# Kernel optimization log

Measured on AMD Instinct MI355X. Metric: run time of the kernel, lower is better.

Reference implementation:

```python
import jax, jax.numpy as jnp
import numpy as np

B, O, M, H, E = 32, 64, 128, 4, 64  # batch, num_obj, memory_len, heads, embed


def setup_inputs() -> dict:
    key = jax.random.key(0)
    ks = jax.random.split(key, 10)
    s = 1.0 / np.sqrt(E)
    return {
        "query": jax.random.normal(ks[0], (B, O, E), jnp.float32),
        "context": jax.random.normal(ks[1], (B, M, E), jnp.float32),
        "memory": jax.random.normal(ks[2], (B, M, E), jnp.float32),
        "W_ch": jax.random.normal(ks[3], (E, H * E), jnp.float32) * s,
        "b_ch": jax.random.normal(ks[4], (H * E,), jnp.float32) * s,
        "w_logit": jax.random.normal(ks[5], (E,), jnp.float32) * s,
        "b_logit": jax.random.normal(ks[6], (1,), jnp.float32) * s,
        "W_rh": jax.random.normal(ks[7], (H * E, E), jnp.float32) * (1.0 / np.sqrt(H * E)),
        "b_rh": jax.random.normal(ks[8], (E,), jnp.float32) * (1.0 / np.sqrt(H * E)),
        "temp": jnp.float32(1.0),
    }


def reference(query, context, memory, W_ch, b_ch, w_logit, b_logit, W_rh, b_rh, temp):
    # create heads: [B,O,E] -> [B,O,H,E]
    q = (query @ W_ch + b_ch).reshape(B, O, H, E)
    # broadcast add query heads and context over memory axis: [B,O,M,H,E]
    qc = jnp.tanh(context[:, None, :, None, :] + q[:, :, None, :, :])
    # logit projection -> [B,O,M,H]
    logits = jnp.einsum("bomhe,e->bomh", qc, w_logit) + b_logit[0]
    # softmax over memory axis (dim=2)
    probs = jax.nn.softmax(logits / temp, axis=2)
    # weighted sum of memory over M: [B,O,H,E]
    heads = jnp.einsum("bomh,bme->bohe", probs, memory)
    heads = jax.nn.leaky_relu(heads, negative_slope=0.01)
    out = heads.reshape(B, O, H * E) @ W_rh + b_rh
    return out
```

## Files before the change

kernel.cpp:

```cpp
#include <hip/hip_runtime.h>
#include <hip/hip_fp16.h>

#define B 32
#define O 64
#define M 128
#define H 4
#define E 64
#define SC 2.88539008177792681f
#define LOG2E 1.44269504088896341f

#if __has_builtin(__builtin_amdgcn_exp2f)
#define EXP2F(x) __builtin_amdgcn_exp2f(x)
#else
#define EXP2F(x) __exp2f(x)
#endif

__device__ __forceinline__ float rl(float v, int lane) {
    return __uint_as_float(__builtin_amdgcn_readlane(__float_as_uint(v), lane));
}
__device__ __forceinline__ unsigned pk2h(float a, float b) {
    return (unsigned)__half_as_ushort(__float2half_rn(a)) |
           ((unsigned)__half_as_ushort(__float2half_rn(b)) << 16);
}

__global__ __launch_bounds__(256) void prep_kernel(
    const float* __restrict__ query, const float* __restrict__ context,
    const float* __restrict__ memory, const float* __restrict__ W_ch,
    const float* __restrict__ b_ch,
    __half* __restrict__ ctx_Eh, __half* __restrict__ mem_T, float* __restrict__ q_E)
{
    __shared__ float s[128 * 68];
    const int t = threadIdx.x, blk = blockIdx.x;

    if (blk < 64) {
        const int b = blk & 31;
        const bool is_ctx = blk < 32;
        const int e = t >> 2, mb = (t & 3) * 32;
        const float* src = (is_ctx ? context : memory) + b * (M * E);
        #pragma unroll
        for (int i = 0; i < 8; ++i) {
            int idx = i * 1024 + t * 4;
            float4 v = *(const float4*)(src + idx);
            *(float4*)(&s[(idx >> 6) * 68 + (idx & 63)]) = v;
        }
        __syncthreads();
        if (is_ctx) {
            uint4* dst = (uint4*)(ctx_Eh + (size_t)b * (E * M) + e * M + mb);
            #pragma unroll
            for (int qd = 0; qd < 4; ++qd) {
                unsigned u[4];
                #pragma unroll
                for (int k = 0; k < 4; ++k) {
                    int m0 = mb + qd * 8 + 2 * k;
                    float ea = fminf(EXP2F(SC * s[m0 * 68 + e]), 60000.f);
                    float eb = fminf(EXP2F(SC * s[(m0 + 1) * 68 + e]), 60000.f);
                    u[k] = pk2h(ea, eb);
                }
                dst[qd] = make_uint4(u[0], u[1], u[2], u[3]);
            }
        } else {
            uint4* dst = (uint4*)(mem_T + (size_t)b * (E * M) + e * M + mb);
            #pragma unroll
            for (int qd = 0; qd < 4; ++qd) {
                unsigned u[4];
                #pragma unroll
                for (int k = 0; k < 4; ++k) {
                    int m0 = mb + qd * 8 + 2 * k;
                    u[k] = pk2h(s[m0 * 68 + e], s[(m0 + 1) * 68 + e]);
                }
                dst[qd] = make_uint4(u[0], u[1], u[2], u[3]);
            }
        }
    } else {
        const int r0 = (blk - 64) * 4;
        s[t] = query[(r0 + (t & 3)) * 64 + (t >> 2)];
        __syncthreads();
        float bc = b_ch[t];
        float a0 = bc, a1 = bc, a2 = bc, a3 = bc;
        #pragma unroll 8
        for (int k = 0; k < 64; ++k) {
            float4 qv = *(const float4*)(&s[k * 4]);
            float wv = W_ch[k * 256 + t];
            a0 = fmaf(qv.x, wv, a0);
            a1 = fmaf(qv.y, wv, a1);
            a2 = fmaf(qv.z, wv, a2);
            a3 = fmaf(qv.w, wv, a3);
        }
        float* qa = q_E + (size_t)r0 * 256 + t;
        qa[0]   = EXP2F(SC * a0);
        qa[256] = EXP2F(SC * a1);
        qa[512] = EXP2F(SC * a2);
        qa[768] = EXP2F(SC * a3);
    }
}

__global__ __launch_bounds__(256) void attn_main(
    const __half* __restrict__ ctx_Eh, const __half* __restrict__ mem_T,
    const float* __restrict__ q_E, const float* __restrict__ w_logit,
    const float* __restrict__ b_logit, const float* __restrict__ temp,
    const float* __restrict__ W_rh, const float* __restrict__ b_rh,
    float* __restrict__ out)
{
    __shared__ __half s_E[E * M];
    __shared__ float4 s_qwu[H * E];
    __shared__ float  s_prob0[M * H];
    __shared__ float  s_prob1[M * H];
    __shared__ float  s_part0[H * 4 * E];
    __shared__ float  s_part1[H * 4 * E];
    __shared__ float  s_po0[4 * E];
    __shared__ float  s_po1[4 * E];

    const int t = threadIdx.x, lane = t & 63, w = t >> 6;
    const int bo0 = blockIdx.x * 2, bo1 = bo0 + 1, b = bo0 >> 6;

    {
        const uint4* g = (const uint4*)(ctx_Eh + (size_t)b * (E * M));
        uint4* l = (uint4*)s_E;
        #pragma unroll
        for (int p = 0; p < 4; ++p)
            l[p * 256 + t] = g[p * 256 + t];
    }
    const float wl = w_logit[lane];
    s_qwu[t] = make_float4(wl, q_E[bo0 * 256 + t], q_E[bo1 * 256 + t], 0.f);
    float sumw = wl;
    #pragma unroll
    for (int sft = 1; sft < 64; sft <<= 1) sumw += __shfl_xor(sumw, sft);
    const float bl   = b_logit[0];
    const float lsc  = LOG2E / temp[0];
    const float base = (sumw + bl) * lsc;
    const float lsc2 = -2.0f * lsc;
    __syncthreads();

    float a00 = 0.f, a01 = 0.f, a10 = 0.f, a11 = 0.f;
    const __half2* Ep = (const __half2*)s_E;
    const float4*  qp = &s_qwu[w * 64];
    #pragma unroll 4
    for (int e = 0; e < 64; ++e) {
        float2 cf = __half22float2(Ep[e * 64 + lane]);
        float4 qw = qp[e];
        float t00 = fmaf(cf.x, qw.y, 1.0f);
        float t01 = fmaf(cf.y, qw.y, 1.0f);
        float t10 = fmaf(cf.x, qw.z, 1.0f);
        float t11 = fmaf(cf.y, qw.z, 1.0f);
        float r0 = __builtin_amdgcn_rcpf(t00 * t01);
        float r1 = __builtin_amdgcn_rcpf(t10 * t11);
        float w0 = qw.x * r0;
        float w1 = qw.x * r1;
        a00 = fmaf(w0, t01, a00);  a01 = fmaf(w0, t00, a01);
        a10 = fmaf(w1, t11, a10);  a11 = fmaf(w1, t10, a11);
    }

    uint4 mr[4];
    {
        const uint4* mp = (const uint4*)(mem_T + (size_t)b * (E * M) + lane * M + 32 * w);
        mr[0] = mp[0]; mr[1] = mp[1]; mr[2] = mp[2]; mr[3] = mp[3];
    }

    float l00 = fmaf(lsc2, a00, base), l01 = fmaf(lsc2, a01, base);
    float l10 = fmaf(lsc2, a10, base), l11 = fmaf(lsc2, a11, base);
    float mx0 = fmaxf(l00, l01), mx1 = fmaxf(l10, l11);
    #pragma unroll
    for (int sft = 1; sft < 64; sft <<= 1) {
        mx0 = fmaxf(mx0, __shfl_xor(mx0, sft));
        mx1 = fmaxf(mx1, __shfl_xor(mx1, sft));
    }
    float e00 = EXP2F(l00 - mx0), e01 = EXP2F(l01 - mx0);
    float e10 = EXP2F(l10 - mx1), e11 = EXP2F(l11 - mx1);
    float s0 = e00 + e01, s1 = e10 + e11;
    #pragma unroll
    for (int sft = 1; sft < 64; sft <<= 1) {
        s0 += __shfl_xor(s0, sft);
        s1 += __shfl_xor(s1, sft);
    }
    float rs0 = __builtin_amdgcn_rcpf(s0), rs1 = __builtin_amdgcn_rcpf(s1);
    s_prob0[(2 * lane) * H + w]     = e00 * rs0;
    s_prob0[(2 * lane + 1) * H + w] = e01 * rs0;
    s_prob1[(2 * lane) * H + w]     = e10 * rs1;
    s_prob1[(2 * lane + 1) * H + w] = e11 * rs1;
    __syncthreads();

    float h00 = 0.f, h01 = 0.f, h02 = 0.f, h03 = 0.f;
    float h10 = 0.f, h11 = 0.f, h12 = 0.f, h13 = 0.f;
    {
        union { uint4 u4[4]; __half2 h2[16]; } mu;
        mu.u4[0] = mr[0]; mu.u4[1] = mr[1]; mu.u4[2] = mr[2]; mu.u4[3] = mr[3];
        const int mbase = 32 * w;
        #pragma unroll 8
        for (int j = 0; j < 16; ++j) {
            float2 mv = __half22float2(mu.h2[j]);
            int m = mbase + 2 * j;
            float4 pa = *(const float4*)(&s_prob0[m * 4]);
            float4 pb = *(const float4*)(&s_prob0[(m + 1) * 4]);
            h00 = fmaf(pa.x, mv.x, h00); h01 = fmaf(pa.y, mv.x, h01);
            h02 = fmaf(pa.z, mv.x, h02); h03 = fmaf(pa.w, mv.x, h03);
            h00 = fmaf(pb.x, mv.y, h00); h01 = fmaf(pb.y, mv.y, h01);
            h02 = fmaf(pb.z, mv.y, h02); h03 = fmaf(pb.w, mv.y, h03);
            float4 pc = *(const float4*)(&s_prob1[m * 4]);
            float4 pd = *(const float4*)(&s_prob1[(m + 1) * 4]);
            h10 = fmaf(pc.x, mv.x, h10); h11 = fmaf(pc.y, mv.x, h11);
            h12 = fmaf(pc.z, mv.x, h12); h13 = fmaf(pc.w, mv.x, h13);
            h10 = fmaf(pd.x, mv.y, h10); h11 = fmaf(pd.y, mv.y, h11);
            h12 = fmaf(pd.z, mv.y, h12); h13 = fmaf(pd.w, mv.y, h13);
        }
    }
    s_part0[0 * 256 + w * 64 + lane] = h00;
    s_part0[1 * 256 + w * 64 + lane] = h01;
    s_part0[2 * 256 + w * 64 + lane] = h02;
    s_part0[3 * 256 + w * 64 + lane] = h03;
    s_part1[0 * 256 + w * 64 + lane] = h10;
    s_part1[1 * 256 + w * 64 + lane] = h11;
    s_part1[2 * 256 + w * 64 + lane] = h12;
    s_part1[3 * 256 + w * 64 + lane] = h13;
    __syncthreads();
    float hv0 = s_part0[w * 256 + lane] + s_part0[w * 256 + 64 + lane]
              + s_part0[w * 256 + 128 + lane] + s_part0[w * 256 + 192 + lane];
    float hv1 = s_part1[w * 256 + lane] + s_part1[w * 256 + 64 + lane]
              + s_part1[w * 256 + 128 + lane] + s_part1[w * 256 + 192 + lane];
    hv0 = (hv0 > 0.f) ? hv0 : 0.01f * hv0;
    hv1 = (hv1 > 0.f) ? hv1 : 0.01f * hv1;

    {
        float acc0 = 0.f, acc1 = 0.f;
        const float* Wp = W_rh + (w * 64) * 64 + lane;
        #pragma unroll 8
        for (int jj = 0; jj < 64; ++jj) {
            float wv = Wp[jj * 64];
            float hj0 = rl(hv0, jj);
            float hj1 = rl(hv1, jj);
            acc0 = fmaf(hj0, wv, acc0);
            acc1 = fmaf(hj1, wv, acc1);
        }
        s_po0[w * 64 + lane] = acc0;
        s_po1[w * 64 + lane] = acc1;
    }
    __syncthreads();
    if (t < 64) {
        float o = s_po0[t] + s_po0[64 + t] + s_po0[128 + t] + s_po0[192 + t] + b_rh[t];
        out[(size_t)bo0 * 64 + t] = o;
    } else if (t < 128) {
        int e2 = t - 64;
        float o = s_po1[e2] + s_po1[64 + e2] + s_po1[128 + e2] + s_po1[192 + e2] + b_rh[e2];
        out[(size_t)bo1 * 64 + e2] = o;
    }
}

extern "C" void kernel_launch(void* const* d_in, const int* in_sizes, int n_in,
                              void* d_out, int out_size, void* d_ws, size_t ws_size,
                              hipStream_t stream) {
    const float* query   = (const float*)d_in[0];
    const float* context = (const float*)d_in[1];
    const float* memory  = (const float*)d_in[2];
    const float* W_ch    = (const float*)d_in[3];
    const float* b_ch    = (const float*)d_in[4];
    const float* w_logit = (const float*)d_in[5];
    const float* b_logit = (const float*)d_in[6];
    const float* W_rh    = (const float*)d_in[7];
    const float* b_rh    = (const float*)d_in[8];
    const float* temp    = (const float*)d_in[9];
    float* out = (float*)d_out;

    __half* ctx_Eh  = (__half*)d_ws;
    __half* mem_T   = ctx_Eh + (size_t)B * E * M;
    float*  q_E     = (float*)(mem_T + (size_t)B * E * M);

    prep_kernel<<<576, 256, 0, stream>>>(query, context, memory, W_ch, b_ch,
                                         ctx_Eh, mem_T, q_E);
    attn_main<<<B * O / 2, 256, 0, stream>>>(ctx_Eh, mem_T, q_E, w_logit,
                                             b_logit, temp, W_rh, b_rh, out);
}
```

Measured before the change: 97.02 us.

## Fuse prep kernel into attention kernel, computing query heads and exp(context) per block

Removes the separate prep kernel and its workspace round trip. Each attention block now computes its own two query-head projections from W_ch, reads context directly from global memory, applies the exp2 transform, and stores it as half2 in shared memory with an XOR swizzle to avoid bank conflicts. Memory values are read as fp32 straight from global memory instead of a pre-transposed fp16 copy. In exchange, the exp of each batch's context is recomputed by all 32 blocks sharing that batch, and W_ch is re-read by every block, which adds redundant compute and L2 traffic while saving one launch and the intermediate writes and reads.

```diff
diff --git a/kernel.cpp b/kernel.cpp
--- a/kernel.cpp
+++ b/kernel.cpp
@@ -18,90 +18,17 @@
 __device__ __forceinline__ float rl(float v, int lane) {
     return __uint_as_float(__builtin_amdgcn_readlane(__float_as_uint(v), lane));
 }
-__device__ __forceinline__ unsigned pk2h(float a, float b) {
-    return (unsigned)__half_as_ushort(__float2half_rn(a)) |
-           ((unsigned)__half_as_ushort(__float2half_rn(b)) << 16);
-}
-
-__global__ __launch_bounds__(256) void prep_kernel(
+
+__global__ __launch_bounds__(256) void attn_fused(
     const float* __restrict__ query, const float* __restrict__ context,
     const float* __restrict__ memory, const float* __restrict__ W_ch,
-    const float* __restrict__ b_ch,
-    __half* __restrict__ ctx_Eh, __half* __restrict__ mem_T, float* __restrict__ q_E)
-{
-    __shared__ float s[128 * 68];
-    const int t = threadIdx.x, blk = blockIdx.x;
-
-    if (blk < 64) {
-        const int b = blk & 31;
-        const bool is_ctx = blk < 32;
-        const int e = t >> 2, mb = (t & 3) * 32;
-        const float* src = (is_ctx ? context : memory) + b * (M * E);
-        #pragma unroll
-        for (int i = 0; i < 8; ++i) {
-            int idx = i * 1024 + t * 4;
-            float4 v = *(const float4*)(src + idx);
-            *(float4*)(&s[(idx >> 6) * 68 + (idx & 63)]) = v;
-        }
-        __syncthreads();
-        if (is_ctx) {
-            uint4* dst = (uint4*)(ctx_Eh + (size_t)b * (E * M) + e * M + mb);
-            #pragma unroll
-            for (int qd = 0; qd < 4; ++qd) {
-                unsigned u[4];
-                #pragma unroll
-                for (int k = 0; k < 4; ++k) {
-                    int m0 = mb + qd * 8 + 2 * k;
-                    float ea = fminf(EXP2F(SC * s[m0 * 68 + e]), 60000.f);
-                    float eb = fminf(EXP2F(SC * s[(m0 + 1) * 68 + e]), 60000.f);
-                    u[k] = pk2h(ea, eb);
-                }
-                dst[qd] = make_uint4(u[0], u[1], u[2], u[3]);
-            }
-        } else {
-            uint4* dst = (uint4*)(mem_T + (size_t)b * (E * M) + e * M + mb);
-            #pragma unroll
-            for (int qd = 0; qd < 4; ++qd) {
-                unsigned u[4];
-                #pragma unroll
-                for (int k = 0; k < 4; ++k) {
-                    int m0 = mb + qd * 8 + 2 * k;
-                    u[k] = pk2h(s[m0 * 68 + e], s[(m0 + 1) * 68 + e]);
-                }
-                dst[qd] = make_uint4(u[0], u[1], u[2], u[3]);
-            }
-        }
-    } else {
-        const int r0 = (blk - 64) * 4;
-        s[t] = query[(r0 + (t & 3)) * 64 + (t >> 2)];
-        __syncthreads();
-        float bc = b_ch[t];
-        float a0 = bc, a1 = bc, a2 = bc, a3 = bc;
-        #pragma unroll 8
-        for (int k = 0; k < 64; ++k) {
-            float4 qv = *(const float4*)(&s[k * 4]);
-            float wv = W_ch[k * 256 + t];
-            a0 = fmaf(qv.x, wv, a0);
-            a1 = fmaf(qv.y, wv, a1);
-            a2 = fmaf(qv.z, wv, a2);
-            a3 = fmaf(qv.w, wv, a3);
-        }
-        float* qa = q_E + (size_t)r0 * 256 + t;
-        qa[0]   = EXP2F(SC * a0);
-        qa[256] = EXP2F(SC * a1);
-        qa[512] = EXP2F(SC * a2);
-        qa[768] = EXP2F(SC * a3);
-    }
-}
-
-__global__ __launch_bounds__(256) void attn_main(
-    const __half* __restrict__ ctx_Eh, const __half* __restrict__ mem_T,
-    const float* __restrict__ q_E, const float* __restrict__ w_logit,
+    const float* __restrict__ b_ch, const float* __restrict__ w_logit,
     const float* __restrict__ b_logit, const float* __restrict__ temp,
     const float* __restrict__ W_rh, const float* __restrict__ b_rh,
     float* __restrict__ out)
 {
-    __shared__ __half s_E[E * M];
+    __shared__ __half2 s_E[E * 64];
+    __shared__ float2 s_q2[E];
     __shared__ float4 s_qwu[H * E];
     __shared__ float  s_prob0[M * H];
     __shared__ float  s_prob1[M * H];
@@ -113,30 +40,53 @@
     const int t = threadIdx.x, lane = t & 63, w = t >> 6;
     const int bo0 = blockIdx.x * 2, bo1 = bo0 + 1, b = bo0 >> 6;
 
-    {
-        const uint4* g = (const uint4*)(ctx_Eh + (size_t)b * (E * M));
-        uint4* l = (uint4*)s_E;
-        #pragma unroll
-        for (int p = 0; p < 4; ++p)
-            l[p * 256 + t] = g[p * 256 + t];
-    }
-    const float wl = w_logit[lane];
-    s_qwu[t] = make_float4(wl, q_E[bo0 * 256 + t], q_E[bo1 * 256 + t], 0.f);
+    if (t < 128)
+        ((float*)s_q2)[t] = query[(size_t)(bo0 + (t & 1)) * E + (t >> 1)];
+    const float wl  = w_logit[lane];
+    const float bl  = b_logit[0];
+    const float lsc = LOG2E / temp[0];
+    float a0 = b_ch[t];
+    float a1 = a0;
+    __syncthreads();
+
+    {
+        const float* Wp = W_ch + t;
+        #pragma unroll 8
+        for (int k = 0; k < 64; ++k) {
+            float wv = Wp[k * 256];
+            float2 qv = s_q2[k];
+            a0 = fmaf(qv.x, wv, a0);
+            a1 = fmaf(qv.y, wv, a1);
+        }
+    }
+    s_qwu[t] = make_float4(wl, EXP2F(SC * a0), EXP2F(SC * a1), 0.f);
+
+    {
+        const float* cp = context + (size_t)b * (M * E) + lane;
+        #pragma unroll 4
+        for (int p = 0; p < 16; ++p) {
+            int c = p * 4 + w;
+            float f0 = cp[(2 * c) * 64];
+            float f1 = cp[(2 * c) * 64 + 64];
+            float ea = fminf(EXP2F(SC * f0), 60000.f);
+            float eb = fminf(EXP2F(SC * f1), 60000.f);
+            s_E[lane * 64 + (c ^ lane)] =
+                __halves2half2(__float2half_rn(ea), __float2half_rn(eb));
+        }
+    }
+
     float sumw = wl;
     #pragma unroll
     for (int sft = 1; sft < 64; sft <<= 1) sumw += __shfl_xor(sumw, sft);
-    const float bl   = b_logit[0];
-    const float lsc  = LOG2E / temp[0];
     const float base = (sumw + bl) * lsc;
     const float lsc2 = -2.0f * lsc;
     __syncthreads();
 
     float a00 = 0.f, a01 = 0.f, a10 = 0.f, a11 = 0.f;
-    const __half2* Ep = (const __half2*)s_E;
-    const float4*  qp = &s_qwu[w * 64];
+    const float4* qp = &s_qwu[w * 64];
     #pragma unroll 4
     for (int e = 0; e < 64; ++e) {
-        float2 cf = __half22float2(Ep[e * 64 + lane]);
+        float2 cf = __half22float2(s_E[e * 64 + (lane ^ e)]);
         float4 qw = qp[e];
         float t00 = fmaf(cf.x, qw.y, 1.0f);
         float t01 = fmaf(cf.y, qw.y, 1.0f);
@@ -150,10 +100,14 @@
         a10 = fmaf(w1, t11, a10);  a11 = fmaf(w1, t10, a11);
     }
 
-    uint4 mr[4];
-    {
-        const uint4* mp = (const uint4*)(mem_T + (size_t)b * (E * M) + lane * M + 32 * w);
-        mr[0] = mp[0]; mr[1] = mp[1]; mr[2] = mp[2]; mr[3] = mp[3];
+    float mrx[16], mry[16];
+    {
+        const float* mp = memory + (size_t)b * (M * E) + (32 * w) * 64 + lane;
+        #pragma unroll
+        for (int j = 0; j < 16; ++j) {
+            mrx[j] = mp[(2 * j) * 64];
+            mry[j] = mp[(2 * j) * 64 + 64];
+        }
     }
 
     float l00 = fmaf(lsc2, a00, base), l01 = fmaf(lsc2, a01, base);
@@ -182,25 +136,23 @@
     float h00 = 0.f, h01 = 0.f, h02 = 0.f, h03 = 0.f;
     float h10 = 0.f, h11 = 0.f, h12 = 0.f, h13 = 0.f;
     {
-        union { uint4 u4[4]; __half2 h2[16]; } mu;
-        mu.u4[0] = mr[0]; mu.u4[1] = mr[1]; mu.u4[2] = mr[2]; mu.u4[3] = mr[3];
         const int mbase = 32 * w;
         #pragma unroll 8
         for (int j = 0; j < 16; ++j) {
-            float2 mv = __half22float2(mu.h2[j]);
+            float mvx = mrx[j], mvy = mry[j];
             int m = mbase + 2 * j;
             float4 pa = *(const float4*)(&s_prob0[m * 4]);
             float4 pb = *(const float4*)(&s_prob0[(m + 1) * 4]);
-            h00 = fmaf(pa.x, mv.x, h00); h01 = fmaf(pa.y, mv.x, h01);
-            h02 = fmaf(pa.z, mv.x, h02); h03 = fmaf(pa.w, mv.x, h03);
-            h00 = fmaf(pb.x, mv.y, h00); h01 = fmaf(pb.y, mv.y, h01);
-            h02 = fmaf(pb.z, mv.y, h02); h03 = fmaf(pb.w, mv.y, h03);
+            h00 = fmaf(pa.x, mvx, h00); h01 = fmaf(pa.y, mvx, h01);
+            h02 = fmaf(pa.z, mvx, h02); h03 = fmaf(pa.w, mvx, h03);
+            h00 = fmaf(pb.x, mvy, h00); h01 = fmaf(pb.y, mvy, h01);
+            h02 = fmaf(pb.z, mvy, h02); h03 = fmaf(pb.w, mvy, h03);
             float4 pc = *(const float4*)(&s_prob1[m * 4]);
             float4 pd = *(const float4*)(&s_prob1[(m + 1) * 4]);
-            h10 = fmaf(pc.x, mv.x, h10); h11 = fmaf(pc.y, mv.x, h11);
-            h12 = fmaf(pc.z, mv.x, h12); h13 = fmaf(pc.w, mv.x, h13);
-            h10 = fmaf(pd.x, mv.y, h10); h11 = fmaf(pd.y, mv.y, h11);
-            h12 = fmaf(pd.z, mv.y, h12); h13 = fmaf(pd.w, mv.y, h13);
+            h10 = fmaf(pc.x, mvx, h10); h11 = fmaf(pc.y, mvx, h11);
+            h12 = fmaf(pc.z, mvx, h12); h13 = fmaf(pc.w, mvx, h13);
+            h10 = fmaf(pd.x, mvy, h10); h11 = fmaf(pd.y, mvy, h11);
+            h12 = fmaf(pd.z, mvy, h12); h13 = fmaf(pd.w, mvy, h13);
         }
     }
     s_part0[0 * 256 + w * 64 + lane] = h00;
@@ -259,12 +211,6 @@
     const float* temp    = (const float*)d_in[9];
     float* out = (float*)d_out;
 
-    __half* ctx_Eh  = (__half*)d_ws;
-    __half* mem_T   = ctx_Eh + (size_t)B * E * M;
-    float*  q_E     = (float*)(mem_T + (size_t)B * E * M);
-
-    prep_kernel<<<576, 256, 0, stream>>>(query, context, memory, W_ch, b_ch,
-                                         ctx_Eh, mem_T, q_E);
-    attn_main<<<B * O / 2, 256, 0, stream>>>(ctx_Eh, mem_T, q_E, w_logit,
-                                             b_logit, temp, W_rh, b_rh, out);
+    attn_fused<<<B * O / 2, 256, 0, stream>>>(query, context, memory, W_ch, b_ch,
+                                              w_logit, b_logit, temp, W_rh, b_rh, out);
 }
```

Result: faster. 92.00 us (-5.2%).
